# Optimization experiments

Measured on AMD Instinct MI355X. Metric: run time of the kernel, lower is better.

## Reference

```python
import jax, jax.numpy as jnp
import numpy as np

H = 768          # hidden_size
V = 512          # vocab_size
NUM_OPS = 64
N_INT = 2        # num_internal_ops
D = 13           # tree depth; complete binary tree
N_NODES = (1 << (D + 1)) - 1  # 16383, level-major layout: level d occupies [2^d-1, 2^(d+1)-1)
TEMP = 3.0


def setup_inputs() -> dict:
    key = jax.random.key(0)
    ks = jax.random.split(key, 24)
    s = 0.02
    nrm = lambda k, shp: jax.random.normal(k, shp, dtype=jnp.float32) * s
    return {
        "ids": jax.random.randint(ks[0], (N_NODES,), 0, V, dtype=jnp.int32),
        "mask": jax.random.randint(ks[1], (N_NODES, NUM_OPS), 0, 2, dtype=jnp.int32),
        # binary Tree-LSTM (N=2), Tai et al. N-ary formulation
        "Wb_iou": nrm(ks[2], (V, 3 * H)), "Ub_iou": nrm(ks[3], (2, H, 3 * H)), "bb_iou": jnp.zeros((3 * H,), jnp.float32),
        "Wb_f": nrm(ks[4], (V, H)), "Ub_f": nrm(ks[5], (2, 2, H, H)), "bb_f": jnp.ones((H,), jnp.float32),
        # ternary Tree-LSTM (N=3)
        "Wt_iou": nrm(ks[6], (V, 3 * H)), "Ut_iou": nrm(ks[7], (3, H, 3 * H)), "bt_iou": jnp.zeros((3 * H,), jnp.float32),
        "Wt_f": nrm(ks[8], (V, H)), "Ut_f": nrm(ks[9], (3, 3, H, H)), "bt_f": jnp.ones((H,), jnp.float32),
        # FFN(H,H,H,n_layers=1): Linear->ReLU->Linear
        "ffn_W1": nrm(ks[10], (H, H)), "ffn_b1": jnp.zeros((H,), jnp.float32),
        "ffn_W2": nrm(ks[11], (H, H)), "ffn_b2": jnp.zeros((H,), jnp.float32),
        # actor heads
        "hl_W": nrm(ks[12], (H, 2)), "hl_b": jnp.zeros((2,), jnp.float32),
        "int_W": nrm(ks[13], (H, N_INT)), "int_b": jnp.zeros((N_INT,), jnp.float32),
        "act_W": nrm(ks[14], (H, NUM_OPS)), "act_b": jnp.zeros((NUM_OPS,), jnp.float32),
    }


def _cell(x_iou, x_f, hc, cc, U_iou, b_iou, U_f, b_f):
    """Batched N-ary Tree-LSTM cell. hc, cc: (n, K, H)."""
    iou = x_iou + jnp.einsum('nkh,kho->no', hc, U_iou) + b_iou
    i, o, g = jnp.split(iou, 3, axis=-1)
    i = jax.nn.sigmoid(i); o = jax.nn.sigmoid(o); g = jnp.tanh(g)
    # per-child forget gate mixes all children hiddens
    f = jax.nn.sigmoid(x_f[:, None, :] + jnp.einsum('nlh,klho->nko', hc, U_f) + b_f)
    c = i * g + jnp.sum(f * cc, axis=1)
    h = o * jnp.tanh(c)
    return h, c


def reference(ids, mask,
              Wb_iou, Ub_iou, bb_iou, Wb_f, Ub_f, bb_f,
              Wt_iou, Ut_iou, bt_iou, Wt_f, Ut_f, bt_f,
              ffn_W1, ffn_b1, ffn_W2, ffn_b2,
              hl_W, hl_b, int_W, int_b, act_W, act_b):
    dt = Wb_iou.dtype
    # ---- apply_binary_lstm: bottom-up, batched per tree level ----
    h_lv = [None] * (D + 1)
    c_lv = [None] * (D + 1)
    for d in range(D, -1, -1):
        n = 1 << d
        off = n - 1
        lid = ids[off:off + n]
        if d == D:  # leaves: missing children -> zero hidden/cell (self.tz)
            hc = jnp.zeros((n, 2, H), dt); cc = jnp.zeros((n, 2, H), dt)
        else:
            hc = h_lv[d + 1].reshape(n, 2, H)
            cc = c_lv[d + 1].reshape(n, 2, H)
        h_lv[d], c_lv[d] = _cell(Wb_iou[lid], Wb_f[lid], hc, cc, Ub_iou, bb_iou, Ub_f, bb_f)
    # ---- internal op 1: apply_ternary_lstm(depth=0) at every node, batched ----
    # uses (own h, child-a h, child-b h); leaves get all zeros (a is None branch)
    h3_parts = []
    for d in range(D + 1):
        n = 1 << d
        off = n - 1
        lid = ids[off:off + n]
        if d == D:
            hc = jnp.zeros((n, 3, H), dt); cc = jnp.zeros((n, 3, H), dt)
        else:
            hc = jnp.concatenate([h_lv[d][:, None, :], h_lv[d + 1].reshape(n, 2, H)], axis=1)
            cc = jnp.concatenate([c_lv[d][:, None, :], c_lv[d + 1].reshape(n, 2, H)], axis=1)
        h3, _ = _cell(Wt_iou[lid], Wt_f[lid], hc, cc, Ut_iou, bt_iou, Ut_f, bt_f)
        h3_parts.append(h3)
    h = jnp.concatenate(h3_parts, axis=0)  # [N_NODES, H], level-major
    # ---- internal op 0: apply_ffn ----
    h = jax.nn.relu(h @ ffn_W1 + ffn_b1) @ ffn_W2 + ffn_b2
    # ---- policy heads (temperature softmaxes, masked actor) ----
    hl = jax.nn.softmax((h @ hl_W + hl_b) / TEMP, axis=-1)
    il = jax.nn.softmax((h @ int_W + int_b) / TEMP, axis=-1)
    mf = mask.astype(dt)
    lin = (h @ act_W + act_b) * mf                       # F.linear with mask-zeroed W, b
    logits = jnp.where(mf > 0, lin, jnp.asarray(-1e30, dt))  # validity_mask.log() + lin
    ap = jax.nn.softmax(logits / TEMP, axis=-1)
    return jnp.concatenate([hl, il, ap], axis=-1)  # [N_NODES, 2 + N_INT + NUM_OPS]
```

## Files before the change

### kernel.cpp

```cpp
#include <hip/hip_runtime.h>
#include <hip/hip_bf16.h>

#define HD 768
#define N_NODES 16383
#define NLEAF_OFF 8191
#define NHF 12582144
#define TEMP 3.0f

using bf16 = __hip_bfloat16;
typedef __attribute__((ext_vector_type(8))) short bf16x8;
typedef __attribute__((ext_vector_type(4))) float f32x4;

__device__ __forceinline__ float sigm(float x) { return 1.0f / (1.0f + __expf(-x)); }
__device__ __forceinline__ float b2f(bf16 v)   { return __bfloat162float(v); }
__device__ __forceinline__ bf16  f2b(float v)  { return __float2bfloat16(v); }

__device__ __forceinline__ void gload16(const void* g, void* l) {
    __builtin_amdgcn_global_load_lds(
        (const __attribute__((address_space(1))) unsigned int*)g,
        (__attribute__((address_space(3))) unsigned int*)l, 16, 0, 0);
}

#define T1SZ 5898240
#define T2SZ 10616832
#define WSZ  589824

__global__ __launch_bounds__(256) void tconv_k(
    const float* __restrict__ Ub_iou, const float* __restrict__ Ub_f,
    const float* __restrict__ Ut_iou, const float* __restrict__ Ut_f,
    const float* __restrict__ ffn_W1,
    bf16* __restrict__ BT1, bf16* __restrict__ BT2, bf16* __restrict__ W1T)
{
    int t = blockIdx.x;
    const float* src; bf16* dst; int C, S, kt, nt;
    if (t < 3456) {
        src = Ub_iou; dst = BT1; C = 2304; S = 1536;
        kt = t % 48; nt = t / 48;
    } else if (t < 5760) {
        int u = t - 3456; int piece = u / 576; u -= piece * 576;
        int kk = piece >> 1, l = piece & 1;
        src = Ub_f + (size_t)(kk * 2 + l) * WSZ;
        dst = BT1 + (size_t)(2304 + kk * 768) * 1536 + l * 768;
        C = 768; S = 1536; kt = u % 24; nt = u / 24;
    } else if (t < 10944) {
        int u = t - 5760;
        src = Ut_iou; dst = BT2; C = 2304; S = 2304;
        kt = u % 72; nt = u / 72;
    } else if (t < 16128) {
        int u = t - 10944; int piece = u / 576; u -= piece * 576;
        int kk = piece / 3, l = piece - kk * 3;
        src = Ut_f + (size_t)(kk * 3 + l) * WSZ;
        dst = BT2 + (size_t)(2304 + kk * 768) * 2304 + l * 768;
        C = 768; S = 2304; kt = u % 24; nt = u / 24;
    } else {
        int u = t - 16128;
        src = ffn_W1; dst = W1T; C = 768; S = 768;
        kt = u % 24; nt = u / 24;
    }
    int k0 = kt * 32, n0 = nt * 32;

    __shared__ float tl[32][33];
    int rr = threadIdx.x >> 5, c = threadIdx.x & 31;
#pragma unroll
    for (int r = 0; r < 32; r += 8)
        tl[rr + r][c] = src[(size_t)(k0 + rr + r) * C + n0 + c];
    __syncthreads();
#pragma unroll
    for (int r = 0; r < 32; r += 8)
        dst[(size_t)(n0 + rr + r) * S + k0 + c] = f2b(tl[c][rr + r]);
}

#define HSZ2 98304
__global__ __launch_bounds__(256) void misc_k(
    const float* __restrict__ hlW, const float* __restrict__ intW,
    const float* __restrict__ actW, const float* __restrict__ W2,
    bf16* __restrict__ WhT, bf16* __restrict__ W2b)
{
    int idx = blockIdx.x * 256 + threadIdx.x;
    if (idx < HSZ2) {
        int n = idx / 768, j = idx - n * 768;
        float v = 0.f;
        if (n < 2)       v = hlW[(size_t)j * 2 + n];
        else if (n < 4)  v = intW[(size_t)j * 2 + (n - 2)];
        else if (n < 68) v = actW[(size_t)j * 64 + (n - 4)];
        WhT[idx] = f2b(v);
    } else if (idx < HSZ2 + WSZ) {
        int i2 = idx - HSZ2;
        W2b[i2] = f2b(W2[i2]);
    }
}

__global__ __launch_bounds__(128) void bck_k(
    const float* __restrict__ b2,
    const float* __restrict__ hlW, const float* __restrict__ hlb,
    const float* __restrict__ intW, const float* __restrict__ intb,
    const float* __restrict__ actW, const float* __restrict__ actb,
    float* __restrict__ bc)
{
    int n = threadIdx.x;
    float s = 0.f;
    for (int j = 0; j < 768; ++j) {
        float wh = 0.f;
        if (n < 2)       wh = hlW[(size_t)j * 2 + n];
        else if (n < 4)  wh = intW[(size_t)j * 2 + (n - 2)];
        else if (n < 68) wh = actW[(size_t)j * 64 + (n - 4)];
        s = fmaf(b2[j], wh, s);
    }
    float hb = 0.f;
    if (n < 2)       hb = hlb[n];
    else if (n < 4)  hb = intb[n - 2];
    else if (n < 68) hb = actb[n - 4];
    bc[n] = s + hb;
}

__global__ __launch_bounds__(256) void leaf_k(
    const int* __restrict__ ids,
    const float* __restrict__ Wb, const float* __restrict__ bb,
    const float* __restrict__ Wt, const float* __restrict__ bt,
    bf16* __restrict__ h_all, bf16* __restrict__ c_all, bf16* __restrict__ h3_all)
{
    int idx = blockIdx.x * blockDim.x + threadIdx.x;
    if (idx >= 8192 * HD) return;
    int i = idx / HD, j = idx - i * HD;
    int g = NLEAF_OFF + i;
    int id = ids[g];
    const float* w = Wb + (size_t)id * 3 * HD;
    float iv = sigm(w[j] + bb[j]);
    float ov = sigm(w[HD + j] + bb[HD + j]);
    float gv = tanhf(w[2 * HD + j] + bb[2 * HD + j]);
    float c = iv * gv;
    h_all[(size_t)g * HD + j] = f2b(ov * tanhf(c));
    c_all[(size_t)g * HD + j] = f2b(c);

    const float* w2 = Wt + (size_t)id * 3 * HD;
    float iv2 = sigm(w2[j] + bt[j]);
    float ov2 = sigm(w2[HD + j] + bt[HD + j]);
    float gv2 = tanhf(w2[2 * HD + j] + bt[2 * HD + j]);
    float c2 = iv2 * gv2;
    h3_all[(size_t)g * HD + j] = f2b(ov2 * tanhf(c2));
}

template <int EPI, int GATHER>
__global__ __launch_bounds__(256) void mm_k(
    const bf16* __restrict__ A, const bf16* __restrict__ BT,
    float* __restrict__ Cf, bf16* __restrict__ Cb,
    const float* __restrict__ bias,
    int M, int N, int Kc, int Kfull)
{
    __shared__ short As[128 * 32];
    __shared__ short Bs[128 * 32];

    int tid  = threadIdx.x;
    int lane = tid & 63;
    int wave = tid >> 6;
    int wr = wave >> 1, wc = wave & 1;
    int bx = blockIdx.x, by = blockIdx.y;
    int colbase = blockIdx.z * Kc;
    if constexpr (EPI == 0) Cf += (size_t)blockIdx.z * ((size_t)M * N);

    f32x4 acc[4][4] = {};

    int sr  = lane >> 2;
    int sc8 = (lane & 3) * 8;
    int arow0 = by * 128 + wave * 16 + sr;
    int arow1 = arow0 + 64;
    if (arow0 > M - 1) arow0 = M - 1;
    if (arow1 > M - 1) arow1 = M - 1;
    const bf16* gA0 = A + (size_t)arow0 * Kfull + colbase + sc8;
    const bf16* gA1 = A + (size_t)arow1 * Kfull + colbase + sc8;
    const bf16* gB0 = BT + (size_t)(bx * 128 + wave * 16 + sr) * Kfull + colbase + sc8;
    const bf16* gB1 = BT + (size_t)(bx * 128 + wave * 16 + sr + 64) * Kfull + colbase + sc8;
    short* lA0 = As + wave * 512;
    short* lA1 = As + wave * 512 + 2048;
    short* lB0 = Bs + wave * 512;
    short* lB1 = Bs + wave * 512 + 2048;

    int fr = lane & 15;
    int fk = (lane >> 4) << 3;
    const short* pAf = As + (wr * 64 + fr) * 32 + fk;
    const short* pBf = Bs + (wc * 64 + fr) * 32 + fk;

    for (int kt = 0; kt < Kc; kt += 32) {
        if constexpr (GATHER) {
            int abs0 = colbase + kt;
            int ch = (abs0 >= 768) + (abs0 >= 1536);
            int col = abs0 - ch * 768 + sc8;
            int n0 = (ch == 0) ? arow0 : (2 * arow0 + ch);
            int n1 = (ch == 0) ? arow1 : (2 * arow1 + ch);
            gload16(A + (size_t)n0 * HD + col, lA0);
            gload16(A + (size_t)n1 * HD + col, lA1);
        } else {
            gload16(gA0 + kt, lA0);
            gload16(gA1 + kt, lA1);
        }
        gload16(gB0 + kt, lB0);
        gload16(gB1 + kt, lB1);
        __syncthreads();

        bf16x8 a[4], b[4];
#pragma unroll
        for (int m = 0; m < 4; m++) a[m] = *(const bf16x8*)(pAf + m * 512);
#pragma unroll
        for (int n = 0; n < 4; n++) b[n] = *(const bf16x8*)(pBf + n * 512);
#pragma unroll
        for (int m = 0; m < 4; m++)
#pragma unroll
            for (int n = 0; n < 4; n++)
                acc[m][n] = __builtin_amdgcn_mfma_f32_16x16x32_bf16(
                    a[m], b[n], acc[m][n], 0, 0, 0);
        __syncthreads();
    }

    int rbase = by * 128 + wr * 64 + ((lane >> 4) << 2);
    int cbase = bx * 128 + wc * 64 + fr;
#pragma unroll
    for (int m = 0; m < 4; m++) {
#pragma unroll
        for (int r = 0; r < 4; r++) {
            int row = rbase + m * 16 + r;
            if (row >= M) continue;
#pragma unroll
            for (int n = 0; n < 4; n++) {
                int col = cbase + n * 16;
                float v = acc[m][n][r];
                if constexpr (EPI == 1) {
                    v = fmaxf(v + bias[col], 0.f);
                    Cb[(size_t)row * N + col] = f2b(v);
                } else if constexpr (EPI == 3) {
                    Cb[(size_t)row * N + col] = f2b(v);
                } else {
                    Cf[(size_t)row * N + col] = v;
                }
            }
        }
    }
}

__global__ __launch_bounds__(256) void cell1_k(
    const int* __restrict__ ids, const bf16* __restrict__ S,
    const float* __restrict__ Wiou, const float* __restrict__ biou,
    const float* __restrict__ Wf, const float* __restrict__ bfv,
    bf16* __restrict__ h_all, bf16* __restrict__ c_all,
    int m, int offAbs)
{
    int idx = blockIdx.x * blockDim.x + threadIdx.x;
    if (idx >= m * HD) return;
    int i = idx / HD, j = idx - i * HD;
    int g = offAbs + i;
    int id = ids[g];
    const bf16* s = S + (size_t)i * 3840;
    const float* w = Wiou + (size_t)id * 2304;
    float iv = sigm(b2f(s[j]) + w[j] + biou[j]);
    float ov = sigm(b2f(s[HD + j]) + w[HD + j] + biou[HD + j]);
    float gv = tanhf(b2f(s[2 * HD + j]) + w[2 * HD + j] + biou[2 * HD + j]);
    float xf = Wf[(size_t)id * HD + j] + bfv[j];
    float f0 = sigm(b2f(s[3 * HD + j]) + xf);
    float f1 = sigm(b2f(s[4 * HD + j]) + xf);
    float c = iv * gv
            + f0 * b2f(c_all[(size_t)(2 * g + 1) * HD + j])
            + f1 * b2f(c_all[(size_t)(2 * g + 2) * HD + j]);
    h_all[(size_t)g * HD + j] = f2b(ov * tanhf(c));
    c_all[(size_t)g * HD + j] = f2b(c);
}

__global__ __launch_bounds__(256) void cell1s_k(
    const int* __restrict__ ids, const float* __restrict__ Sf,
    const float* __restrict__ Wiou, const float* __restrict__ biou,
    const float* __restrict__ Wf, const float* __restrict__ bfv,
    bf16* __restrict__ h_all, bf16* __restrict__ c_all,
    int m, int offAbs, int KS)
{
    int idx = blockIdx.x * blockDim.x + threadIdx.x;
    if (idx >= m * HD) return;
    int i = idx / HD, j = idx - i * HD;
    int g = offAbs + i;
    int id = ids[g];
    const float* s = Sf + (size_t)i * 3840;
    size_t zs = (size_t)m * 3840;
    float si = 0.f, so = 0.f, su = 0.f, p0 = 0.f, p1 = 0.f;
    for (int z = 0; z < KS; ++z) {
        const float* sz = s + z * zs;
        si += sz[j];
        so += sz[HD + j];
        su += sz[2 * HD + j];
        p0 += sz[3 * HD + j];
        p1 += sz[4 * HD + j];
    }
    const float* w = Wiou + (size_t)id * 2304;
    float iv = sigm(si + w[j] + biou[j]);
    float ov = sigm(so + w[HD + j] + biou[HD + j]);
    float gv = tanhf(su + w[2 * HD + j] + biou[2 * HD + j]);
    float xf = Wf[(size_t)id * HD + j] + bfv[j];
    float f0 = sigm(p0 + xf);
    float f1 = sigm(p1 + xf);
    float c = iv * gv
            + f0 * b2f(c_all[(size_t)(2 * g + 1) * HD + j])
            + f1 * b2f(c_all[(size_t)(2 * g + 2) * HD + j]);
    h_all[(size_t)g * HD + j] = f2b(ov * tanhf(c));
    c_all[(size_t)g * HD + j] = f2b(c);
}

__global__ __launch_bounds__(256) void cell2_k(
    const int* __restrict__ ids, const bf16* __restrict__ S,
    const float* __restrict__ Wiou, const float* __restrict__ biou,
    const float* __restrict__ Wf, const float* __restrict__ bfv,
    const bf16* __restrict__ c_all, bf16* __restrict__ h3_all,
    int m, int g0)
{
    int idx = blockIdx.x * blockDim.x + threadIdx.x;
    if (idx >= m * HD) return;
    int i = idx / HD, j = idx - i * HD;
    int g = g0 + i;
    int id = ids[g];
    const bf16* s = S + (size_t)i * 4608;
    const float* w = Wiou + (size_t)id * 2304;
    float iv = sigm(b2f(s[j]) + w[j] + biou[j]);
    float ov = sigm(b2f(s[HD + j]) + w[HD + j] + biou[HD + j]);
    float gv = tanhf(b2f(s[2 * HD + j]) + w[2 * HD + j] + biou[2 * HD + j]);
    float xf = Wf[(size_t)id * HD + j] + bfv[j];
    float f0 = sigm(b2f(s[3 * HD + j]) + xf);
    float f1 = sigm(b2f(s[4 * HD + j]) + xf);
    float f2 = sigm(b2f(s[5 * HD + j]) + xf);
    float c = iv * gv
            + f0 * b2f(c_all[(size_t)g * HD + j])
            + f1 * b2f(c_all[(size_t)(2 * g + 1) * HD + j])
            + f2 * b2f(c_all[(size_t)(2 * g + 2) * HD + j]);
    h3_all[(size_t)g * HD + j] = f2b(ov * tanhf(c));
}

__global__ __launch_bounds__(256) void hsm_k(
    const float* __restrict__ L, const int* __restrict__ mask,
    const float* __restrict__ bc, float* __restrict__ out)
{
    int g = blockIdx.x * 4 + (threadIdx.x >> 6);
    if (g >= N_NODES) return;
    int t = threadIdx.x & 63;
    const float* lr = L + (size_t)g * 128;

    bool on = mask[(size_t)g * 64 + t] > 0;
    float x = (lr[4 + t] + bc[4 + t]) * (1.0f / TEMP);
    float mx = on ? x : -INFINITY;
#pragma unroll
    for (int o = 32; o; o >>= 1) mx = fmaxf(mx, __shfl_xor(mx, o));
    float e = on ? __expf(x - mx) : 0.0f;
    float s = e;
#pragma unroll
    for (int o = 32; o; o >>= 1) s += __shfl_xor(s, o);
    float r = (s > 0.f) ? e / s : (1.0f / 64.0f);
    out[(size_t)g * 68 + 4 + t] = r;

    if (t == 0) {
        float a = (lr[0] + bc[0]) * (1.0f / TEMP);
        float b = (lr[1] + bc[1]) * (1.0f / TEMP);
        float m2 = fmaxf(a, b);
        float e0 = __expf(a - m2), e1 = __expf(b - m2);
        out[(size_t)g * 68 + 0] = e0 / (e0 + e1);
        out[(size_t)g * 68 + 1] = e1 / (e0 + e1);
    } else if (t == 1) {
        float a = (lr[2] + bc[2]) * (1.0f / TEMP);
        float b = (lr[3] + bc[3]) * (1.0f / TEMP);
        float m2 = fmaxf(a, b);
        float e0 = __expf(a - m2), e1 = __expf(b - m2);
        out[(size_t)g * 68 + 2] = e0 / (e0 + e1);
        out[(size_t)g * 68 + 3] = e1 / (e0 + e1);
    }
}

extern "C" void kernel_launch(void* const* d_in, const int* in_sizes, int n_in,
                              void* d_out, int out_size, void* d_ws, size_t ws_size,
                              hipStream_t stream)
{
    const int*   ids     = (const int*)d_in[0];
    const int*   mask    = (const int*)d_in[1];
    const float* Wb_iou  = (const float*)d_in[2];
    const float* Ub_iou  = (const float*)d_in[3];
    const float* bb_iou  = (const float*)d_in[4];
    const float* Wb_f    = (const float*)d_in[5];
    const float* Ub_f    = (const float*)d_in[6];
    const float* bb_f    = (const float*)d_in[7];
    const float* Wt_iou  = (const float*)d_in[8];
    const float* Ut_iou  = (const float*)d_in[9];
    const float* bt_iou  = (const float*)d_in[10];
    const float* Wt_f    = (const float*)d_in[11];
    const float* Ut_f    = (const float*)d_in[12];
    const float* bt_f    = (const float*)d_in[13];
    const float* ffn_W1  = (const float*)d_in[14];
    const float* ffn_b1  = (const float*)d_in[15];
    const float* ffn_W2  = (const float*)d_in[16];
    const float* ffn_b2  = (const float*)d_in[17];
    const float* hl_W    = (const float*)d_in[18];
    const float* hl_b    = (const float*)d_in[19];
    const float* int_W   = (const float*)d_in[20];
    const float* int_b   = (const float*)d_in[21];
    const float* act_W   = (const float*)d_in[22];
    const float* act_b   = (const float*)d_in[23];

    char* p = (char*)d_ws;
    bf16* h_all  = (bf16*)p; p += (size_t)NHF * 2;
    bf16* c_all  = (bf16*)p; p += (size_t)NHF * 2;
    bf16* h3_all = (bf16*)p; p += (size_t)NHF * 2;
    bf16* BT1 = (bf16*)p; p += (size_t)T1SZ * 2;
    bf16* BT2 = (bf16*)p; p += (size_t)T2SZ * 2;
    bf16* W1T = (bf16*)p; p += (size_t)WSZ * 2;
    bf16* WcT = (bf16*)p; p += (size_t)128 * 768 * 2;
    bf16* WhT = (bf16*)p; p += (size_t)HSZ2 * 2;
    bf16* W2b = (bf16*)p; p += (size_t)WSZ * 2;
    float* bc = (float*)p; p += 512;
    bf16* Sb  = (bf16*)p;
    float* Sf = (float*)Sb;
    bf16* t1  = c_all;
    float* Lg = (float*)h3_all;

    tconv_k<<<16704, 256, 0, stream>>>(
        Ub_iou, Ub_f, Ut_iou, Ut_f, ffn_W1, BT1, BT2, W1T);
    misc_k<<<(HSZ2 + WSZ + 255) / 256, 256, 0, stream>>>(
        hl_W, int_W, act_W, ffn_W2, WhT, W2b);
    bck_k<<<1, 128, 0, stream>>>(
        ffn_b2, hl_W, hl_b, int_W, int_b, act_W, act_b, bc);
    mm_k<3, 0><<<dim3(6, 1), 256, 0, stream>>>(
        WhT, W2b, nullptr, WcT, nullptr, 128, 768, 768, 768);

    leaf_k<<<(8192 * HD + 255) / 256, 256, 0, stream>>>(
        ids, Wb_iou, bb_iou, Wt_iou, bt_iou, h_all, c_all, h3_all);

    for (int d = 12; d >= 0; --d) {
        int n = 1 << d;
        int childoff = 2 * n - 1;
        if (n >= 512) {
            mm_k<3, 0><<<dim3(30, n / 128), 256, 0, stream>>>(
                h_all + (size_t)childoff * HD, BT1, nullptr, Sb, nullptr,
                n, 3840, 1536, 1536);
            cell1_k<<<(n * HD + 255) / 256, 256, 0, stream>>>(
                ids, Sb, Wb_iou, bb_iou, Wb_f, bb_f, h_all, c_all, n, n - 1);
        } else {
            mm_k<0, 0><<<dim3(30, (n + 127) / 128, 6), 256, 0, stream>>>(
                h_all + (size_t)childoff * HD, BT1, Sf, nullptr, nullptr,
                n, 3840, 256, 1536);
            cell1s_k<<<(n * HD + 255) / 256, 256, 0, stream>>>(
                ids, Sf, Wb_iou, bb_iou, Wb_f, bb_f, h_all, c_all, n, n - 1, 6);
        }
    }

    mm_k<3, 1><<<dim3(36, 64), 256, 0, stream>>>(
        h_all, BT2, nullptr, Sb, nullptr, NLEAF_OFF, 4608, 2304, 2304);
    cell2_k<<<(NLEAF_OFF * HD + 255) / 256, 256, 0, stream>>>(
        ids, Sb, Wt_iou, bt_iou, Wt_f, bt_f, c_all, h3_all, NLEAF_OFF, 0);

    mm_k<1, 0><<<dim3(6, 128), 256, 0, stream>>>(
        h3_all, W1T, nullptr, t1, ffn_b1, N_NODES, 768, 768, 768);

    mm_k<0, 0><<<dim3(1, 128), 256, 0, stream>>>(
        t1, WcT, Lg, nullptr, nullptr, N_NODES, 128, 768, 768);
    hsm_k<<<(N_NODES + 3) / 4, 256, 0, stream>>>(
        Lg, mask, bc, (float*)d_out);
}
```

Before: 842.0 us.

## Add 256x256-tile 8-wave pipelined GEMM for large tree levels and ternary pass

Result: slower. 872.6 us (+3.6%).

```diff
diff --git a/kernel.cpp b/kernel.cpp
--- a/kernel.cpp
+++ b/kernel.cpp
@@ -140,6 +140,131 @@
     h3_all[(size_t)g * HD + j] = f2b(ov2 * tanhf(c2));
 }
 
+template <int GATHER>
+__global__ __launch_bounds__(512, 2) void mm8_k(
+    const bf16* __restrict__ A, const bf16* __restrict__ BT,
+    bf16* __restrict__ Cb, int M, int N, int K)
+{
+    __shared__ short Al[2][16384];
+    __shared__ short Bl[2][16384];
+
+    const int tid  = threadIdx.x;
+    const int lane = tid & 63;
+    const int wid  = tid >> 6;
+    const int wr = wid >> 2, wc = wid & 3;
+    const int bx = blockIdx.x, by = blockIdx.y;
+    const int NT = K >> 6;
+
+    const int srow = wid * 8 + (lane >> 3);
+    const int scol = (lane & 7) * 8;
+    const int frow = lane & 15;
+    const int fks  = (lane >> 4) * 8;
+
+    f32x4 acc[8][4] = {};
+
+    auto stageA = [&](int t, int cr) {
+        int slot = t & 1;
+        int grow = by * 256 + cr + srow;
+        if (grow > M - 1) grow = M - 1;
+        int kb = t * 64;
+        const bf16* src;
+        if constexpr (GATHER) {
+            int ch = kb / 768;
+            int node = (ch == 0) ? grow : (2 * grow + ch);
+            src = A + (size_t)node * 768 + (kb - ch * 768) + scol;
+        } else {
+            src = A + (size_t)grow * K + kb + scol;
+        }
+        gload16(src, &Al[slot][(cr + wid * 8) * 64]);
+    };
+    auto stageB = [&](int t, int cr) {
+        int slot = t & 1;
+        const bf16* src = BT + (size_t)(bx * 256 + cr + srow) * K + t * 64 + scol;
+        gload16(src, &Bl[slot][(cr + wid * 8) * 64]);
+    };
+
+    stageB(0, 0);   stageB(0, 64);
+    stageB(0, 128); stageB(0, 192);
+    stageA(0, 0);   stageA(0, 128);
+    stageA(0, 64);  stageA(0, 192);
+    stageB(1, 0);   stageB(1, 64);
+    stageB(1, 128); stageB(1, 192);
+    stageA(1, 0);   stageA(1, 128);
+    asm volatile("s_waitcnt vmcnt(6)" ::: "memory");
+    __builtin_amdgcn_s_barrier();
+
+#define PHASE(Q, STAGES, TAILWAIT)                                           \
+    {                                                                        \
+        bf16x8 a[2][2];                                                      \
+        _Pragma("unroll")                                                    \
+        for (int mq = 0; mq < 2; ++mq)                                       \
+            _Pragma("unroll")                                                \
+            for (int ks = 0; ks < 2; ++ks)                                   \
+                a[mq][ks] = *(const bf16x8*)&Ax[                             \
+                    (wr * 128 + ((Q) * 2 + mq) * 16 + frow) * 64 + ks * 32 + fks]; \
+        STAGES;                                                              \
+        __builtin_amdgcn_s_barrier();                                        \
+        asm volatile("s_waitcnt lgkmcnt(0)" ::: "memory");                   \
+        __builtin_amdgcn_sched_barrier(0);                                   \
+        __builtin_amdgcn_s_setprio(1);                                       \
+        _Pragma("unroll")                                                    \
+        for (int mq = 0; mq < 2; ++mq)                                       \
+            _Pragma("unroll")                                                \
+            for (int nf = 0; nf < 4; ++nf)                                   \
+                _Pragma("unroll")                                            \
+                for (int ks = 0; ks < 2; ++ks)                               \
+                    acc[(Q) * 2 + mq][nf] =                                  \
+                        __builtin_amdgcn_mfma_f32_16x16x32_bf16(             \
+                            a[mq][ks], b[nf][ks], acc[(Q) * 2 + mq][nf], 0, 0, 0); \
+        __builtin_amdgcn_s_setprio(0);                                       \
+        TAILWAIT;                                                            \
+        __builtin_amdgcn_s_barrier();                                        \
+    }
+
+    for (int t = 0; t < NT; ++t) {
+        short* Ax = Al[t & 1];
+        short* Bx = Bl[t & 1];
+        bf16x8 b[4][2];
+#pragma unroll
+        for (int nf = 0; nf < 4; ++nf)
+#pragma unroll
+            for (int ks = 0; ks < 2; ++ks)
+                b[nf][ks] = *(const bf16x8*)&Bx[
+                    (wc * 64 + nf * 16 + frow) * 64 + ks * 32 + fks];
+
+        PHASE(0,
+              { if (t + 1 < NT) { stageA(t + 1, 64); stageA(t + 1, 192); } },
+              {})
+        PHASE(1,
+              { if (t + 2 < NT) { stageB(t + 2, 0); stageB(t + 2, 64); } },
+              {})
+        PHASE(2,
+              { if (t + 2 < NT) { stageB(t + 2, 128); stageB(t + 2, 192); } },
+              {})
+        PHASE(3,
+              { if (t + 2 < NT) { stageA(t + 2, 0); stageA(t + 2, 128); } },
+              {
+                  if (t + 2 < NT) asm volatile("s_waitcnt vmcnt(6)" ::: "memory");
+                  else            asm volatile("s_waitcnt vmcnt(0)" ::: "memory");
+              })
+    }
+#undef PHASE
+
+#pragma unroll
+    for (int mf = 0; mf < 8; ++mf) {
+#pragma unroll
+        for (int r = 0; r < 4; ++r) {
+            int row = by * 256 + wr * 128 + mf * 16 + (lane >> 4) * 4 + r;
+            if (row >= M) continue;
+#pragma unroll
+            for (int nf = 0; nf < 4; ++nf) {
+                int col = bx * 256 + wc * 64 + nf * 16 + (lane & 15);
+                Cb[(size_t)row * N + col] = f2b(acc[mf][nf][r]);
+            }
+        }
+    }
+}
+
 template <int EPI, int GATHER>
 __global__ __launch_bounds__(256) void mm_k(
     const bf16* __restrict__ A, const bf16* __restrict__ BT,
@@ -426,7 +551,12 @@
     for (int d = 12; d >= 0; --d) {
         int n = 1 << d;
         int childoff = 2 * n - 1;
-        if (n >= 512) {
+        if (n >= 2048) {
+            mm8_k<0><<<dim3(15, n / 256), 512, 0, stream>>>(
+                h_all + (size_t)childoff * HD, BT1, Sb, n, 3840, 1536);
+            cell1_k<<<(n * HD + 255) / 256, 256, 0, stream>>>(
+                ids, Sb, Wb_iou, bb_iou, Wb_f, bb_f, h_all, c_all, n, n - 1);
+        } else if (n >= 512) {
             mm_k<3, 0><<<dim3(30, n / 128), 256, 0, stream>>>(
                 h_all + (size_t)childoff * HD, BT1, nullptr, Sb, nullptr,
                 n, 3840, 1536, 1536);
@@ -441,8 +571,8 @@
         }
     }
 
-    mm_k<3, 1><<<dim3(36, 64), 256, 0, stream>>>(
-        h_all, BT2, nullptr, Sb, nullptr, NLEAF_OFF, 4608, 2304, 2304);
+    mm8_k<1><<<dim3(18, 32), 512, 0, stream>>>(
+        h_all, BT2, Sb, NLEAF_OFF, 4608, 2304);
     cell2_k<<<(NLEAF_OFF * HD + 255) / 256, 256, 0, stream>>>(
         ids, Sb, Wt_iou, bt_iou, Wt_f, bt_f, c_all, h3_all, NLEAF_OFF, 0);
 
```
